# Optimization experiments

Measured on AMD Instinct MI355X. Metric: run time of the kernel, lower is better.

## Reference

```python
import jax, jax.numpy as jnp
import numpy as np

S, B, N, K, D, H = 4, 8, 2048, 16, 32, 128


def setup_inputs() -> dict:
    key = jax.random.key(0)
    ks = jax.random.split(key, 7)
    x = jax.random.normal(ks[0], (S, B, N, D), dtype=jnp.float32)
    mu = jax.random.normal(ks[1], (S, B, K, D), dtype=jnp.float32)
    tau = jax.random.uniform(ks[2], (S, B, K, D), dtype=jnp.float32)  # precisions > 0
    # Linear(3D -> H); stored as (3D, H) i.e. transpose of torch's (H, 3D) weight
    W1 = jax.random.normal(ks[3], (3 * D, H), dtype=jnp.float32) * (1.0 / np.sqrt(3 * D))
    b1 = jax.random.normal(ks[4], (H,), dtype=jnp.float32) * 0.01
    W2 = jax.random.normal(ks[5], (H, 1), dtype=jnp.float32) * (1.0 / np.sqrt(H))
    b2 = jax.random.normal(ks[6], (1,), dtype=jnp.float32) * 0.01
    return {"x": x, "mu": mu, "tau": tau, "W1": W1, "b1": b1, "W2": W2, "b2": b2}


def reference(x, mu, tau, W1, b1, W2, b2):
    # Original torch code materializes var = cat([x_expand, mu_expand, tau_expand], -1)
    # of shape (S,B,N,K,3D) then applies Linear(3D,H). Mathematically identical:
    # split W1 rows into the x / mu / tau blocks and add the partial projections,
    # which avoids building the (S,B,N,K,3D) concat tensor.
    d = x.shape[-1]
    Wx, Wm, Wt = W1[:d], W1[d:2 * d], W1[2 * d:]
    hx = jnp.einsum('sbnd,dh->sbnh', x, Wx)                       # (S,B,N,H)
    hk = jnp.einsum('sbkd,dh->sbkh', mu, Wm) \
       + jnp.einsum('sbkd,dh->sbkh', tau, Wt)                     # (S,B,K,H)
    h = jnp.tanh(hx[:, :, :, None, :] + hk[:, :, None, :, :] + b1)  # (S,B,N,K,H)
    gamma = jnp.einsum('sbnkh,h->sbnk', h, W2[:, 0]) + b2[0]        # (S,B,N,K)
    q_probs = jax.nn.softmax(gamma, axis=-1)
    return q_probs
```

## Files before the change

### kernel.cpp

```cpp
#include <hip/hip_runtime.h>
#include <math.h>

typedef _Float16 half_t;
typedef __attribute__((ext_vector_type(8))) _Float16 half8;

#define EXP2F(x) __builtin_amdgcn_exp2f(x)
#define RCPF(x)  __builtin_amdgcn_rcpf(x)
#define C_SCALE 2.8853900817779268f

__global__ __launch_bounds__(256) void prep_kernel(
    const float* __restrict__ mu, const float* __restrict__ tau,
    const float* __restrict__ W1, const float* __restrict__ b1,
    const float* __restrict__ W2,
    half_t* __restrict__ ek, half_t* __restrict__ w2h) {
  int g = blockIdx.x * 256 + threadIdx.x;
  int h = g & 127, row = g >> 7;
  const float* mur  = mu  + row * 32;
  const float* taur = tau + row * 32;
  float acc = b1[h];
#pragma unroll
  for (int d = 0; d < 32; ++d) {
    acc = fmaf(mur[d],  W1[(32 + d) * 128 + h], acc);
    acc = fmaf(taur[d], W1[(64 + d) * 128 + h], acc);
  }
  ek[g] = (half_t)EXP2F(C_SCALE * acc);
  if (g < 128) w2h[g] = (half_t)(-2.0f * W2[g]);
}

__global__ __launch_bounds__(256, 3) void main_kernel(
    const float* __restrict__ x, const float* __restrict__ W1,
    const half_t* __restrict__ ek, const half_t* __restrict__ w2h,
    float* __restrict__ out) {
  __shared__ __align__(16) float  sX[64][36];
  __shared__ __align__(16) float  sW[32][132];
  __shared__ __align__(16) half_t sEx[64][136];
  __shared__ __align__(16) half_t sEk[16][136];
  __shared__ __align__(16) half_t sW2[128];

  int t = threadIdx.x;
  int row0 = blockIdx.x * 64;
  int sb = row0 >> 11;

  const float4* x4 = (const float4*)(x + (size_t)row0 * 32);
#pragma unroll
  for (int i = 0; i < 2; ++i) {
    int j = i * 256 + t;
    int n = j >> 3, d4 = j & 7;
    *(float4*)&sX[n][d4 * 4] = x4[j];
  }
  const float4* w4 = (const float4*)W1;
#pragma unroll
  for (int i = 0; i < 4; ++i) {
    int j = i * 256 + t;
    int d = j >> 5, h4 = j & 31;
    float4 v = w4[j];
    v.x *= C_SCALE; v.y *= C_SCALE; v.z *= C_SCALE; v.w *= C_SCALE;
    *(float4*)&sW[d][h4 * 4] = v;
  }
  {
    const float4* ek4 = (const float4*)(ek + (size_t)sb * 2048);
    int k = t >> 4, h8 = t & 15;
    *(float4*)&sEk[k][h8 * 8] = ek4[t];
  }
  if (t < 16) *(float4*)&sW2[t * 8] = ((const float4*)w2h)[t];
  __syncthreads();

  {
    int hg = t & 15, rg = t >> 4;
    int h0 = hg * 8, r0 = rg * 4;
    float acc[4][8];
#pragma unroll
    for (int j = 0; j < 4; ++j)
#pragma unroll
      for (int l = 0; l < 8; ++l) acc[j][l] = 0.f;
#pragma unroll 4
    for (int d = 0; d < 32; ++d) {
      float4 wa = *(const float4*)&sW[d][h0];
      float4 wb = *(const float4*)&sW[d][h0 + 4];
      float w[8] = {wa.x, wa.y, wa.z, wa.w, wb.x, wb.y, wb.z, wb.w};
#pragma unroll
      for (int j = 0; j < 4; ++j) {
        float xv = sX[r0 + j][d];
#pragma unroll
        for (int l = 0; l < 8; ++l) acc[j][l] = fmaf(xv, w[l], acc[j][l]);
      }
    }
#pragma unroll
    for (int j = 0; j < 4; ++j) {
      half8 hv;
#pragma unroll
      for (int l = 0; l < 8; ++l) hv[l] = (half_t)EXP2F(acc[j][l]);
      *(half8*)&sEx[r0 + j][h0] = hv;
    }
  }
  __syncthreads();

  int kg = t & 7, rg = t >> 3;
  int r0 = rg * 2, k0 = kg * 2;
  float a00 = 0.f, a01 = 0.f, a10 = 0.f, a11 = 0.f;
#pragma unroll 2
  for (int h8 = 0; h8 < 16; ++h8) {
    half8 ex0 = *(const half8*)&sEx[r0][h8 * 8];
    half8 ex1 = *(const half8*)&sEx[r0 + 1][h8 * 8];
    half8 ekv0 = *(const half8*)&sEk[k0][h8 * 8];
    half8 ekv1 = *(const half8*)&sEk[k0 + 1][h8 * 8];
    half8 wv = *(const half8*)&sW2[h8 * 8];
#pragma unroll
    for (int j = 0; j < 8; ++j) {
      float e0 = (float)ex0[j], e1 = (float)ex1[j];
      float f0 = (float)ekv0[j], f1 = (float)ekv1[j];
      float w = (float)wv[j];
      a00 = fmaf(w, RCPF(fmaf(e0, f0, 1.0f)), a00);
      a01 = fmaf(w, RCPF(fmaf(e0, f1, 1.0f)), a01);
      a10 = fmaf(w, RCPF(fmaf(e1, f0, 1.0f)), a10);
      a11 = fmaf(w, RCPF(fmaf(e1, f1, 1.0f)), a11);
    }
  }

  const float l2e = 1.4426950408889634f;
  {
    float m = fmaxf(a00, a01);
#pragma unroll
    for (int s = 1; s < 8; s <<= 1) m = fmaxf(m, __shfl_xor(m, s, 8));
    float p0 = EXP2F((a00 - m) * l2e), p1 = EXP2F((a01 - m) * l2e);
    float sum = p0 + p1;
#pragma unroll
    for (int s = 1; s < 8; s <<= 1) sum += __shfl_xor(sum, s, 8);
    float inv = RCPF(sum);
    float2 o = make_float2(p0 * inv, p1 * inv);
    *(float2*)&out[(size_t)(row0 + r0) * 16 + k0] = o;
  }
  {
    float m = fmaxf(a10, a11);
#pragma unroll
    for (int s = 1; s < 8; s <<= 1) m = fmaxf(m, __shfl_xor(m, s, 8));
    float p0 = EXP2F((a10 - m) * l2e), p1 = EXP2F((a11 - m) * l2e);
    float sum = p0 + p1;
#pragma unroll
    for (int s = 1; s < 8; s <<= 1) sum += __shfl_xor(sum, s, 8);
    float inv = RCPF(sum);
    float2 o = make_float2(p0 * inv, p1 * inv);
    *(float2*)&out[(size_t)(row0 + r0 + 1) * 16 + k0] = o;
  }
}

extern "C" void kernel_launch(void* const* d_in, const int* in_sizes, int n_in,
                              void* d_out, int out_size, void* d_ws, size_t ws_size,
                              hipStream_t stream) {
  const float* x   = (const float*)d_in[0];
  const float* mu  = (const float*)d_in[1];
  const float* tau = (const float*)d_in[2];
  const float* W1  = (const float*)d_in[3];
  const float* b1  = (const float*)d_in[4];
  const float* W2  = (const float*)d_in[5];
  float* out = (float*)d_out;

  half_t* ek  = (half_t*)d_ws;
  half_t* w2h = ek + 512 * 128;
  (void)in_sizes; (void)n_in; (void)out_size; (void)ws_size;

  prep_kernel<<<256, 256, 0, stream>>>(mu, tau, W1, b1, W2, ek, w2h);
  main_kernel<<<1024, 256, 0, stream>>>(x, W1, ek, w2h, out);
}
```

Baseline: 92.52 us.

## Rewrite main kernel as register-resident per-thread rows with packed fp32 math

Replaces the shared-memory two-phase kernel (x·W GEMM tile, then fp16 pairwise sigmoid sum) with a kernel where each thread holds two x rows in registers and loops over its 32-slice of H. It computes the projection, exp and reciprocal sum on the fly with packed v2f FMAs, reading pre-transposed, pre-scaled W and transposed ek from global/L1. Partial sums are combined with cross-lane shuffles. The prep kernel now also emits transposed scaled W1 and fp32 ek/w2, dropping fp16. This removes LDS traffic and barriers, but recomputes loads per h from cache and adds register pressure.

Measured after the change: 182.1 us. 1.97x slower.

```diff
diff --git a/kernel.cpp b/kernel.cpp
--- a/kernel.cpp
+++ b/kernel.cpp
@@ -1,18 +1,28 @@
 #include <hip/hip_runtime.h>
 #include <math.h>
 
-typedef _Float16 half_t;
-typedef __attribute__((ext_vector_type(8))) _Float16 half8;
+typedef float v2f __attribute__((ext_vector_type(2)));
 
 #define EXP2F(x) __builtin_amdgcn_exp2f(x)
 #define RCPF(x)  __builtin_amdgcn_rcpf(x)
 #define C_SCALE 2.8853900817779268f
+#define L2E 1.4426950408889634f
+
+#if __has_builtin(__builtin_elementwise_fma)
+static __device__ __forceinline__ v2f fma2(v2f a, v2f b, v2f c) {
+  return __builtin_elementwise_fma(a, b, c);
+}
+#else
+static __device__ __forceinline__ v2f fma2(v2f a, v2f b, v2f c) {
+  v2f r; r.x = fmaf(a.x, b.x, c.x); r.y = fmaf(a.y, b.y, c.y); return r;
+}
+#endif
 
 __global__ __launch_bounds__(256) void prep_kernel(
     const float* __restrict__ mu, const float* __restrict__ tau,
     const float* __restrict__ W1, const float* __restrict__ b1,
     const float* __restrict__ W2,
-    half_t* __restrict__ ek, half_t* __restrict__ w2h) {
+    float* __restrict__ ekT, float* __restrict__ WTc, float* __restrict__ w2n) {
   int g = blockIdx.x * 256 + threadIdx.x;
   int h = g & 127, row = g >> 7;
   const float* mur  = mu  + row * 32;
@@ -23,124 +33,106 @@
     acc = fmaf(mur[d],  W1[(32 + d) * 128 + h], acc);
     acc = fmaf(taur[d], W1[(64 + d) * 128 + h], acc);
   }
-  ek[g] = (half_t)EXP2F(C_SCALE * acc);
-  if (g < 128) w2h[g] = (half_t)(-2.0f * W2[g]);
+  int sb = row >> 4, k = row & 15;
+  ekT[sb * 2048 + h * 16 + k] = EXP2F(C_SCALE * acc);
+  if (g < 4096) {
+    int hh = g >> 5, d = g & 31;
+    WTc[g] = C_SCALE * W1[d * 128 + hh];
+  }
+  if (g < 128) w2n[g] = -2.0f * W2[g];
 }
 
-__global__ __launch_bounds__(256, 3) void main_kernel(
-    const float* __restrict__ x, const float* __restrict__ W1,
-    const half_t* __restrict__ ek, const half_t* __restrict__ w2h,
+__global__ __launch_bounds__(256, 4) void main_kernel(
+    const float* __restrict__ x, const float* __restrict__ WTc,
+    const float* __restrict__ ekT, const float* __restrict__ w2n,
     float* __restrict__ out) {
-  __shared__ __align__(16) float  sX[64][36];
-  __shared__ __align__(16) float  sW[32][132];
-  __shared__ __align__(16) half_t sEx[64][136];
-  __shared__ __align__(16) half_t sEk[16][136];
-  __shared__ __align__(16) half_t sW2[128];
+  int t = threadIdx.x;
+  int hg = t & 3, rp = t >> 2;
+  int row0 = blockIdx.x * 128;
+  int sb = row0 >> 11;
+  int r0 = row0 + rp * 2;
 
-  int t = threadIdx.x;
-  int row0 = blockIdx.x * 64;
-  int sb = row0 >> 11;
-
-  const float4* x4 = (const float4*)(x + (size_t)row0 * 32);
+  v2f xr[2][16];
 #pragma unroll
-  for (int i = 0; i < 2; ++i) {
-    int j = i * 256 + t;
-    int n = j >> 3, d4 = j & 7;
-    *(float4*)&sX[n][d4 * 4] = x4[j];
-  }
-  const float4* w4 = (const float4*)W1;
+  for (int rr = 0; rr < 2; ++rr) {
+    const float4* xp = (const float4*)(x + (size_t)(r0 + rr) * 32);
 #pragma unroll
-  for (int i = 0; i < 4; ++i) {
-    int j = i * 256 + t;
-    int d = j >> 5, h4 = j & 31;
-    float4 v = w4[j];
-    v.x *= C_SCALE; v.y *= C_SCALE; v.z *= C_SCALE; v.w *= C_SCALE;
-    *(float4*)&sW[d][h4 * 4] = v;
-  }
-  {
-    const float4* ek4 = (const float4*)(ek + (size_t)sb * 2048);
-    int k = t >> 4, h8 = t & 15;
-    *(float4*)&sEk[k][h8 * 8] = ek4[t];
-  }
-  if (t < 16) *(float4*)&sW2[t * 8] = ((const float4*)w2h)[t];
-  __syncthreads();
-
-  {
-    int hg = t & 15, rg = t >> 4;
-    int h0 = hg * 8, r0 = rg * 4;
-    float acc[4][8];
-#pragma unroll
-    for (int j = 0; j < 4; ++j)
-#pragma unroll
-      for (int l = 0; l < 8; ++l) acc[j][l] = 0.f;
-#pragma unroll 4
-    for (int d = 0; d < 32; ++d) {
-      float4 wa = *(const float4*)&sW[d][h0];
-      float4 wb = *(const float4*)&sW[d][h0 + 4];
-      float w[8] = {wa.x, wa.y, wa.z, wa.w, wb.x, wb.y, wb.z, wb.w};
-#pragma unroll
-      for (int j = 0; j < 4; ++j) {
-        float xv = sX[r0 + j][d];
-#pragma unroll
-        for (int l = 0; l < 8; ++l) acc[j][l] = fmaf(xv, w[l], acc[j][l]);
-      }
-    }
-#pragma unroll
-    for (int j = 0; j < 4; ++j) {
-      half8 hv;
-#pragma unroll
-      for (int l = 0; l < 8; ++l) hv[l] = (half_t)EXP2F(acc[j][l]);
-      *(half8*)&sEx[r0 + j][h0] = hv;
-    }
-  }
-  __syncthreads();
-
-  int kg = t & 7, rg = t >> 3;
-  int r0 = rg * 2, k0 = kg * 2;
-  float a00 = 0.f, a01 = 0.f, a10 = 0.f, a11 = 0.f;
-#pragma unroll 2
-  for (int h8 = 0; h8 < 16; ++h8) {
-    half8 ex0 = *(const half8*)&sEx[r0][h8 * 8];
-    half8 ex1 = *(const half8*)&sEx[r0 + 1][h8 * 8];
-    half8 ekv0 = *(const half8*)&sEk[k0][h8 * 8];
-    half8 ekv1 = *(const half8*)&sEk[k0 + 1][h8 * 8];
-    half8 wv = *(const half8*)&sW2[h8 * 8];
-#pragma unroll
-    for (int j = 0; j < 8; ++j) {
-      float e0 = (float)ex0[j], e1 = (float)ex1[j];
-      float f0 = (float)ekv0[j], f1 = (float)ekv1[j];
-      float w = (float)wv[j];
-      a00 = fmaf(w, RCPF(fmaf(e0, f0, 1.0f)), a00);
-      a01 = fmaf(w, RCPF(fmaf(e0, f1, 1.0f)), a01);
-      a10 = fmaf(w, RCPF(fmaf(e1, f0, 1.0f)), a10);
-      a11 = fmaf(w, RCPF(fmaf(e1, f1, 1.0f)), a11);
+    for (int i = 0; i < 8; ++i) {
+      float4 v = xp[i];
+      xr[rr][2 * i]     = (v2f){v.x, v.y};
+      xr[rr][2 * i + 1] = (v2f){v.z, v.w};
     }
   }
 
-  const float l2e = 1.4426950408889634f;
-  {
-    float m = fmaxf(a00, a01);
+  const v2f* Wp  = (const v2f*)WTc;
+  const v2f* ekp = (const v2f*)(ekT + (size_t)sb * 2048);
+
+  v2f acc[2][8];
 #pragma unroll
-    for (int s = 1; s < 8; s <<= 1) m = fmaxf(m, __shfl_xor(m, s, 8));
-    float p0 = EXP2F((a00 - m) * l2e), p1 = EXP2F((a01 - m) * l2e);
-    float sum = p0 + p1;
+  for (int rr = 0; rr < 2; ++rr)
 #pragma unroll
-    for (int s = 1; s < 8; s <<= 1) sum += __shfl_xor(sum, s, 8);
+    for (int j = 0; j < 8; ++j) acc[rr][j] = (v2f){0.f, 0.f};
+
+  int h0 = hg * 32;
+#pragma unroll 1
+  for (int hh = 0; hh < 32; ++hh) {
+    int h = h0 + hh;
+    v2f w[16];
+    const v2f* wrow = Wp + h * 16;
+#pragma unroll
+    for (int i = 0; i < 16; ++i) w[i] = wrow[i];
+    v2f ek2[8];
+    const v2f* ekh = ekp + h * 8;
+#pragma unroll
+    for (int j = 0; j < 8; ++j) ek2[j] = ekh[j];
+    float w2 = w2n[h];
+
+    float ex[2];
+#pragma unroll
+    for (int rr = 0; rr < 2; ++rr) {
+      v2f p = (v2f){0.f, 0.f};
+#pragma unroll
+      for (int i = 0; i < 16; ++i) p = fma2(xr[rr][i], w[i], p);
+      ex[rr] = EXP2F(p.x + p.y);
+    }
+#pragma unroll
+    for (int rr = 0; rr < 2; ++rr) {
+      v2f exd = (v2f){ex[rr], ex[rr]};
+#pragma unroll
+      for (int j = 0; j < 8; ++j) {
+        v2f tt = fma2(exd, ek2[j], (v2f){1.f, 1.f});
+        v2f rv = (v2f){RCPF(tt.x), RCPF(tt.y)};
+        acc[rr][j] = fma2((v2f){w2, w2}, rv, acc[rr][j]);
+      }
+    }
+  }
+
+#pragma unroll
+  for (int m = 1; m <= 2; m <<= 1) {
+#pragma unroll
+    for (int rr = 0; rr < 2; ++rr)
+#pragma unroll
+      for (int j = 0; j < 8; ++j) {
+        acc[rr][j].x += __shfl_xor(acc[rr][j].x, m);
+        acc[rr][j].y += __shfl_xor(acc[rr][j].y, m);
+      }
+  }
+
+#pragma unroll
+  for (int rr = 0; rr < 2; ++rr) {
+    float g[16];
+#pragma unroll
+    for (int j = 0; j < 8; ++j) { g[2 * j] = acc[rr][j].x; g[2 * j + 1] = acc[rr][j].y; }
+    float mx = g[0];
+#pragma unroll
+    for (int k = 1; k < 16; ++k) mx = fmaxf(mx, g[k]);
+    float p[16], sum = 0.f;
+#pragma unroll
+    for (int k = 0; k < 16; ++k) { p[k] = EXP2F((g[k] - mx) * L2E); sum += p[k]; }
     float inv = RCPF(sum);
-    float2 o = make_float2(p0 * inv, p1 * inv);
-    *(float2*)&out[(size_t)(row0 + r0) * 16 + k0] = o;
-  }
-  {
-    float m = fmaxf(a10, a11);
-#pragma unroll
-    for (int s = 1; s < 8; s <<= 1) m = fmaxf(m, __shfl_xor(m, s, 8));
-    float p0 = EXP2F((a10 - m) * l2e), p1 = EXP2F((a11 - m) * l2e);
-    float sum = p0 + p1;
-#pragma unroll
-    for (int s = 1; s < 8; s <<= 1) sum += __shfl_xor(sum, s, 8);
-    float inv = RCPF(sum);
-    float2 o = make_float2(p0 * inv, p1 * inv);
-    *(float2*)&out[(size_t)(row0 + r0 + 1) * 16 + k0] = o;
+    float4 o = {p[hg * 4] * inv, p[hg * 4 + 1] * inv,
+                p[hg * 4 + 2] * inv, p[hg * 4 + 3] * inv};
+    *(float4*)&out[(size_t)(r0 + rr) * 16 + hg * 4] = o;
   }
 }
 
@@ -155,10 +147,11 @@
   const float* W2  = (const float*)d_in[5];
   float* out = (float*)d_out;
 
-  half_t* ek  = (half_t*)d_ws;
-  half_t* w2h = ek + 512 * 128;
+  float* ekT = (float*)d_ws;
+  float* WTc = ekT + 32 * 2048;
+  float* w2n = WTc + 4096;
   (void)in_sizes; (void)n_in; (void)out_size; (void)ws_size;
 
-  prep_kernel<<<256, 256, 0, stream>>>(mu, tau, W1, b1, W2, ek, w2h);
-  main_kernel<<<1024, 256, 0, stream>>>(x, W1, ek, w2h, out);
+  prep_kernel<<<256, 256, 0, stream>>>(mu, tau, W1, b1, W2, ekT, WTc, w2n);
+  main_kernel<<<512, 256, 0, stream>>>(x, WTc, ekT, w2n, out);
 }
```
